# Optimization experiments

Hardware: AMD Instinct MI355X
Metric: run time of the kernel (lower is better)

The kernel has to match this reference:

```python
import jax, jax.numpy as jnp
import numpy as np

B, T, K = 128, 1024, 24
START_TAG, END_TAG = 22, 23


def setup_inputs() -> dict:
    key = jax.random.key(0)
    k1, k2, k3 = jax.random.split(key, 3)
    scores = jax.random.normal(k1, (B, T, K, K), dtype=jnp.float32)
    targets = jax.random.randint(k2, (B, T), 0, K * K)
    # lengths must be sorted descending (pack_padded_sequence convention), >= 1
    lengths = jnp.sort(jax.random.randint(k3, (B,), 1, T + 1))[::-1]
    return {"scores": scores, "targets": targets, "lengths": lengths}


def reference(scores, targets, lengths):
    b, t_len, k, _ = scores.shape
    # gold path score: gather targets from flattened [B,T,K*K] view, mask by length
    flat = scores.reshape(b, t_len, k * k)
    scores_at_targets = jnp.take_along_axis(flat, targets[:, :, None], axis=2)[..., 0]  # [B,T]
    time_mask = jnp.arange(t_len)[None, :] < lengths[:, None]  # [B,T]
    gold_score = jnp.sum(jnp.where(time_mask, scores_at_targets, 0.0))

    # CRF forward recursion (log-sum-exp over previous tag), sequential over time.
    # t == 0: initialize with row of the <start> tag (all lengths >= 1).
    prev = scores[:, 0, START_TAG, :]  # [B,K]

    def step(prev, inp):
        s_t, m_t = inp  # s_t: [B,K,K], m_t: [B] bool (t < length)
        new = jax.scipy.special.logsumexp(s_t + prev[:, :, None], axis=1)  # [B,K]
        prev = jnp.where(m_t[:, None], new, prev)
        return prev, None

    s_rest = jnp.moveaxis(scores[:, 1:], 0, 1)  # time-major [T-1,B,K,K]
    m_rest = jnp.arange(1, t_len)[:, None] < lengths[None, :]  # [T-1,B]
    prev, _ = jax.lax.scan(step, prev, (s_rest, m_rest))

    all_paths_scores = prev[:, END_TAG].sum()
    return (all_paths_scores - gold_score) / b
```

## Files before the change

kernel.cpp:

```cpp
#include <hip/hip_runtime.h>

static constexpr int T_LEN = 1024;
static constexpr int KTAG = 24;
static constexpr int MAT = 576;
static constexpr int START_TAG = 22;
static constexpr int END_TAG = 23;
static constexpr int BATCH = 128;
static constexpr int CHUNK = 32;
static constexpr int NCHUNK = 32;

static constexpr float LOG2E = 1.4426950408889634f;
static constexpr float LN2   = 0.6931471805599453f;

typedef short  bf16x8 __attribute__((ext_vector_type(8)));
typedef float  f32x16 __attribute__((ext_vector_type(16)));

__device__ __forceinline__ float fexp2(float x) { return __builtin_amdgcn_exp2f(x); }
__device__ __forceinline__ float flog2(float x) { return __builtin_amdgcn_logf(x); }

__device__ __forceinline__ unsigned int f2bf(float x) {
  unsigned int u = __float_as_uint(x);
  u += 0x7FFFu + ((u >> 16) & 1u);
  return u >> 16;
}

__global__ __launch_bounds__(256) void chunkprod_kernel(
    const float* __restrict__ scores, const int* __restrict__ targets,
    const int* __restrict__ lengths,
    float* __restrict__ wsP, int* __restrict__ wsE, float* __restrict__ wsG)
{
  const int widx = threadIdx.x >> 6;
  const int lane = threadIdx.x & 63;
  const int i = blockIdx.x * 4 + widx;
  const int pr = i >> 1;
  const int anti = i & 1;
  const int b0 = pr >> 4;
  const int c0 = pr & 15;
  const int b = anti ? (127 - b0) : b0;
  const int c = anti ? (31 - c0) : c0;
  const int len = lengths[b];
  const int t0 = 1 + c * CHUNK;
  if (t0 >= len) return;
  const int n = min(CHUNK, len - t0);
  const int hd = lane >> 5;
  const int m = lane & 31;
  const int mc = m < KTAG ? m : KTAG - 1;
  const float* sb = scores + (size_t)b * T_LEN * MAT;

  {
    float gs = 0.f;
    if (lane < n) {
      int t = t0 + lane;
      gs = sb[(size_t)t * MAT + targets[b * T_LEN + t]];
    }
    #pragma unroll
    for (int off = 1; off < 64; off <<= 1) gs += __shfl_xor(gs, off, 64);
    if (lane == 0) wsG[b * NCHUNK + c] = gs;
  }

  int off1[8], off2[4];
  #pragma unroll
  for (int e = 0; e < 8; ++e) {
    int k = (e & 3) + 8 * (e >> 2) + 4 * hd;
    off1[e] = k * KTAG + mc;
  }
  #pragma unroll
  for (int e = 0; e < 4; ++e) {
    int k = 16 + e + 4 * hd;
    off2[e] = k * KTAG + mc;
  }

  float b0r[12], b1r[12], b2r[12], b3r[12];
  auto LOADA = [&](float (&buf)[12], int step) {
    const float* pb = sb + (size_t)(t0 + step) * MAT;
    #pragma unroll
    for (int e = 0; e < 8; ++e) buf[e] = pb[off1[e]];
    #pragma unroll
    for (int e = 0; e < 4; ++e) buf[8 + e] = pb[off2[e]];
  };

  unsigned int p[8];
  #pragma unroll
  for (int r = 0; r < 8; ++r) {
    int rlo = ((2 * r) & 3) + 8 * ((2 * r) >> 2) + 4 * hd;
    unsigned int v = 0;
    if (m == rlo)     v |= 0x3F80u;
    if (m == rlo + 1) v |= (0x3F80u << 16);
    p[r] = v;
  }

  int E = 0;

  auto STEPM = [&](const float (&buf)[12]) -> f32x16 {
    float av[12];
    #pragma unroll
    for (int i2 = 0; i2 < 12; ++i2) av[i2] = fexp2(buf[i2] * LOG2E);
    bf16x8 a1, a2;
    #pragma unroll
    for (int e = 0; e < 8; ++e) a1[e] = (short)f2bf(av[e]);
    #pragma unroll
    for (int e = 0; e < 4; ++e) a2[e] = (short)f2bf(av[8 + e]);
    #pragma unroll
    for (int e = 4; e < 8; ++e) a2[e] = 0;
    union { unsigned int u[4]; bf16x8 v; } B1, B2;
    B1.u[0] = p[0]; B1.u[1] = p[1]; B1.u[2] = p[2]; B1.u[3] = p[3];
    B2.u[0] = p[4]; B2.u[1] = p[5]; B2.u[2] = p[6]; B2.u[3] = p[7];
    f32x16 d = {};
    d = __builtin_amdgcn_mfma_f32_32x32x16_bf16(a1, B1.v, d, 0, 0, 0);
    d = __builtin_amdgcn_mfma_f32_32x32x16_bf16(a2, B2.v, d, 0, 0, 0);
    return d;
  };

  auto CONV = [&](const f32x16& d) {
    int rb = __builtin_amdgcn_readfirstlane(__float_as_int(d[0]));
    int dd = ((rb >> 23) & 255) - 127;
    E += dd;
    float sc = __int_as_float((127 - dd) << 23);
    #pragma unroll
    for (int r = 0; r < 8; ++r)
      p[r] = (f2bf(d[2 * r + 1] * sc) << 16) | f2bf(d[2 * r] * sc);
  };

  LOADA(b0r, 0);
  LOADA(b1r, n > 1 ? 1 : 0);
  LOADA(b2r, n > 2 ? 2 : 0);
  LOADA(b3r, n > 3 ? 3 : 0);
  f32x16 z;
  int s = 0;
  for (;;) {
    z = STEPM(b0r);
    if (s + 1 >= n) break;
    CONV(z); { int t = s + 4; LOADA(b0r, t < n ? t : n - 1); }
    z = STEPM(b1r);
    if (s + 2 >= n) break;
    CONV(z); { int t = s + 5; LOADA(b1r, t < n ? t : n - 1); }
    z = STEPM(b2r);
    if (s + 3 >= n) break;
    CONV(z); { int t = s + 6; LOADA(b2r, t < n ? t : n - 1); }
    z = STEPM(b3r);
    if (s + 4 >= n) break;
    CONV(z); { int t = s + 7; LOADA(b3r, t < n ? t : n - 1); }
    s += 4;
  }

  if (m < KTAG) {
    float* dst = wsP + (size_t)(b * NCHUNK + c) * MAT + m * KTAG;
    float4 v0 = make_float4(z[0], z[1], z[2],  z[3]);
    float4 v1 = make_float4(z[4], z[5], z[6],  z[7]);
    float4 v2 = make_float4(z[8], z[9], z[10], z[11]);
    *(float4*)(dst + 4 * hd)      = v0;
    *(float4*)(dst + 8 + 4 * hd)  = v1;
    *(float4*)(dst + 16 + 4 * hd) = v2;
  }
  if (lane == 0) wsE[b * NCHUNK + c] = E;
}

__global__ __launch_bounds__(64) void chainmat_kernel(
    const float* __restrict__ scores, const int* __restrict__ targets,
    const float* __restrict__ wsP, const int* __restrict__ wsE,
    const float* __restrict__ wsG, const int* __restrict__ lengths,
    float* __restrict__ wsR)
{
  const int b = blockIdx.x;
  const int lane = threadIdx.x;
  const int hd = lane >> 5;
  const int m = lane & 31;
  const int mc = m < KTAG ? m : KTAG - 1;
  const int len = lengths[b];
  const int nc = (len + 30) >> 5;
  const float* sb = scores + (size_t)b * T_LEN * MAT;

  float gv = 0.f;
  if (lane < nc) gv = wsG[b * NCHUNK + lane];
  #pragma unroll
  for (int off = 1; off < 64; off <<= 1) gv += __shfl_xor(gv, off, 64);
  const float g0 = sb[targets[b * T_LEN]];

  if (nc == 0) {
    if (lane == 0) wsR[b] = sb[START_TAG * KTAG + END_TAG] - g0;
    return;
  }

  int ev = 0;
  if (lane < nc) ev = wsE[b * NCHUNK + lane];
  #pragma unroll
  for (int off = 1; off < 64; off <<= 1) ev += __shfl_xor(ev, off, 64);
  int E = ev;

  int off1[8], off2[4];
  #pragma unroll
  for (int e = 0; e < 8; ++e) {
    int k = (e & 3) + 8 * (e >> 2) + 4 * hd;
    off1[e] = k * KTAG + mc;
  }
  #pragma unroll
  for (int e = 0; e < 4; ++e) {
    int k = 16 + e + 4 * hd;
    off2[e] = k * KTAG + mc;
  }
  const float* pbase = wsP + (size_t)b * NCHUNK * MAT;

  float b0[12], b1[12];
  auto LOADP = [&](float (&buf)[12], int c) {
    const float* pb = pbase + (size_t)c * MAT;
    #pragma unroll
    for (int e = 0; e < 8; ++e) buf[e] = pb[off1[e]];
    #pragma unroll
    for (int e = 0; e < 4; ++e) buf[8 + e] = pb[off2[e]];
  };

  unsigned int p[8];
  #pragma unroll
  for (int r = 0; r < 8; ++r) {
    int rlo = ((2 * r) & 3) + 8 * ((2 * r) >> 2) + 4 * hd;
    unsigned int v = 0;
    if (m == rlo)     v |= 0x3F80u;
    if (m == rlo + 1) v |= (0x3F80u << 16);
    p[r] = v;
  }

  auto STEPP = [&](const float (&buf)[12]) -> f32x16 {
    bf16x8 a1, a2;
    #pragma unroll
    for (int e = 0; e < 8; ++e) a1[e] = (short)f2bf(buf[e]);
    #pragma unroll
    for (int e = 0; e < 4; ++e) a2[e] = (short)f2bf(buf[8 + e]);
    #pragma unroll
    for (int e = 4; e < 8; ++e) a2[e] = 0;
    union { unsigned int u[4]; bf16x8 v; } B1, B2;
    B1.u[0] = p[0]; B1.u[1] = p[1]; B1.u[2] = p[2]; B1.u[3] = p[3];
    B2.u[0] = p[4]; B2.u[1] = p[5]; B2.u[2] = p[6]; B2.u[3] = p[7];
    f32x16 d = {};
    d = __builtin_amdgcn_mfma_f32_32x32x16_bf16(a1, B1.v, d, 0, 0, 0);
    d = __builtin_amdgcn_mfma_f32_32x32x16_bf16(a2, B2.v, d, 0, 0, 0);
    return d;
  };
  auto CONVP = [&](const f32x16& d) {
    int rb = __builtin_amdgcn_readfirstlane(__float_as_int(d[0]));
    int dd = ((rb >> 23) & 255) - 127;
    E += dd;
    float sc = __int_as_float((127 - dd) << 23);
    #pragma unroll
    for (int r = 0; r < 8; ++r)
      p[r] = (f2bf(d[2 * r + 1] * sc) << 16) | f2bf(d[2 * r] * sc);
  };

  LOADP(b0, 0);
  LOADP(b1, nc > 1 ? 1 : 0);
  f32x16 z;
  int c = 0;
  for (;;) {
    z = STEPP(b0);
    if (c + 1 >= nc) break;
    CONVP(z); { int t = c + 2; LOADP(b0, t < nc ? t : nc - 1); }
    z = STEPP(b1);
    if (c + 2 >= nc) break;
    CONVP(z); { int t = c + 3; LOADP(b1, t < nc ? t : nc - 1); }
    c += 2;
  }

  float tau0 = fexp2(sb[START_TAG * KTAG + mc] * LOG2E);
  float v = (hd == 1 && m < KTAG) ? z[11] * tau0 : 0.f;
  #pragma unroll
  for (int off = 1; off < 64; off <<= 1) v += __shfl_xor(v, off, 64);
  if (lane == 0) {
    float logZ = ((float)E + flog2(v)) * LN2;
    wsR[b] = logZ - gv - g0;
  }
}

__global__ __launch_bounds__(64) void sum_kernel(
    const float* __restrict__ wsR, float* __restrict__ out)
{
  const int lane = threadIdx.x;
  float v = wsR[lane] + wsR[lane + 64];
  #pragma unroll
  for (int off = 1; off < 64; off <<= 1) v += __shfl_xor(v, off, 64);
  if (lane == 0) out[0] = v * (1.0f / (float)BATCH);
}

template<int DIR>
__device__ __forceinline__ int run_chain(const float* __restrict__ base, int len, int n,
                                         volatile float* __restrict__ tau,
                                         int lane, int h, int jj)
{
  int E = 0;
  float ref = 1.0f;
  float A[12], B[12], Cb[12];
  auto LOAD = [&](float (&buf)[12], int i) {
    if (DIR == 0) {
      const float* p = base + (size_t)(1 + i) * MAT + h * 12 * KTAG + jj;
      #pragma unroll
      for (int k = 0; k < 12; ++k) buf[k] = p[k * KTAG];
    } else {
      const float4* p = (const float4*)(base + (size_t)(len - 1 - i) * MAT + jj * KTAG + h * 12);
      float4 x = p[0], y = p[1], z = p[2];
      buf[0]=x.x; buf[1]=x.y; buf[2]=x.z; buf[3]=x.w;
      buf[4]=y.x; buf[5]=y.y; buf[6]=y.z; buf[7]=y.w;
      buf[8]=z.x; buf[9]=z.y; buf[10]=z.z; buf[11]=z.w;
    }
  };
  auto STEP = [&](const float (&buf)[12]) {
    int rb = __builtin_amdgcn_readfirstlane(__float_as_int(ref));
    int d = ((rb >> 23) & 255) - 127;
    float sc = __int_as_float((127 - d) << 23);
    E += d;
    float w[12];
    #pragma unroll
    for (int k = 0; k < 12; ++k) w[k] = fexp2(buf[k] * LOG2E);
    const float4* tp = (const float4*)((const float*)&tau[h * 12]);
    float4 t0 = tp[0], t1 = tp[1], t2 = tp[2];
    float a0 = t0.x*w[0], a1 = t0.y*w[1], a2 = t0.z*w[2], a3 = t0.w*w[3];
    a0 = fmaf(t1.x, w[4],  a0); a1 = fmaf(t1.y, w[5],  a1);
    a2 = fmaf(t1.z, w[6],  a2); a3 = fmaf(t1.w, w[7],  a3);
    a0 = fmaf(t2.x, w[8],  a0); a1 = fmaf(t2.y, w[9],  a1);
    a2 = fmaf(t2.z, w[10], a2); a3 = fmaf(t2.w, w[11], a3);
    float part = (a0 + a1) + (a2 + a3);
    float tot = part + __shfl_xor(part, 32, 64);
    float tn = tot * sc;
    if (lane < KTAG) tau[lane] = tn;
    ref = tn;
  };
  if (n > 0) {
    LOAD(A, 0); LOAD(B, n > 1 ? 1 : 0); LOAD(Cb, n > 2 ? 2 : 0);
    int i = 0;
    while (i + 3 <= n) {
      STEP(A);  { int ii = i + 3; LOAD(A,  ii < n ? ii : n - 1); }
      STEP(B);  { int ii = i + 4; LOAD(B,  ii < n ? ii : n - 1); }
      STEP(Cb); { int ii = i + 5; LOAD(Cb, ii < n ? ii : n - 1); }
      i += 3;
    }
    if (i < n)     STEP(A);
    if (i + 1 < n) STEP(B);
  }
  return E;
}

__global__ __launch_bounds__(128) void crf_fb_kernel(
    const float* __restrict__ scores, const int* __restrict__ lengths,
    float* __restrict__ acc)
{
  __shared__ float sm[2][32];
  __shared__ int smE[2];
  const int b = blockIdx.x;
  const int tid = threadIdx.x;
  const int wid = tid >> 6;
  const int lane = tid & 63;
  const int h = lane >> 5;
  const int j = lane & 31;
  const int jj = j < KTAG ? j : KTAG - 1;
  const int len = lengths[b];
  const float* base = scores + (size_t)b * T_LEN * MAT;
  const int m = len >> 1;
  volatile float* tau = sm[wid];
  int E;
  if (wid == 0) {
    if (lane < KTAG) tau[lane] = fexp2(base[START_TAG * KTAG + lane] * LOG2E);
    E = run_chain<0>(base, len, m, tau, lane, h, jj);
  } else {
    if (lane < KTAG) tau[lane] = (lane == END_TAG) ? 1.0f : 0.0f;
    E = run_chain<1>(base, len, len - 1 - m, tau, lane, h, jj);
  }
  if (lane == 0) smE[wid] = E;
  __syncthreads();
  if (wid == 0) {
    float v = (lane < KTAG) ? sm[0][lane] * sm[1][lane] : 0.0f;
    #pragma unroll
    for (int off = 1; off < 32; off <<= 1) v += __shfl_xor(v, off, 64);
    if (lane == 0) {
      float res = ((float)(smE[0] + smE[1]) + flog2(v)) * LN2;
      atomicAdd(acc, res);
    }
  }
}

__global__ __launch_bounds__(256) void gold_kernel(
    const float* __restrict__ scores, const int* __restrict__ targets,
    const int* __restrict__ lengths, float* __restrict__ acc)
{
  const int idx = blockIdx.x * blockDim.x + threadIdx.x;
  const int b = idx >> 10;
  const int t = idx & (T_LEN - 1);
  float v = 0.f;
  if (t < lengths[b]) v = scores[(size_t)idx * MAT + targets[idx]];
  #pragma unroll
  for (int off = 1; off < 64; off <<= 1) v += __shfl_xor(v, off, 64);
  if ((threadIdx.x & 63) == 0) atomicAdd(acc, -v);
}

__global__ void finalize_kernel(const float* __restrict__ acc, float* __restrict__ out) {
  out[0] = acc[0] * (1.0f / (float)BATCH);
}

extern "C" void kernel_launch(void* const* d_in, const int* in_sizes, int n_in,
                              void* d_out, int out_size, void* d_ws, size_t ws_size,
                              hipStream_t stream) {
  const float* scores = (const float*)d_in[0];
  const int* targets  = (const int*)d_in[1];
  const int* lengths  = (const int*)d_in[2];
  float* out = (float*)d_out;

  const size_t pbytes = (size_t)BATCH * NCHUNK * MAT * sizeof(float);
  const size_t ebytes = (size_t)BATCH * NCHUNK * sizeof(int);
  const size_t gbytes = (size_t)BATCH * NCHUNK * sizeof(float);
  const size_t need = pbytes + ebytes + gbytes + BATCH * sizeof(float);

  if (ws_size >= need) {
    float* wsP = (float*)d_ws;
    int*   wsE = (int*)((char*)d_ws + pbytes);
    float* wsG = (float*)((char*)d_ws + pbytes + ebytes);
    float* wsR = (float*)((char*)d_ws + pbytes + ebytes + gbytes);
    chunkprod_kernel<<<BATCH * NCHUNK / 4, 256, 0, stream>>>(scores, targets, lengths,
                                                             wsP, wsE, wsG);
    chainmat_kernel<<<BATCH, 64, 0, stream>>>(scores, targets, wsP, wsE, wsG,
                                              lengths, wsR);
    sum_kernel<<<1, 64, 0, stream>>>(wsR, out);
  } else {
    float* acc = (float*)d_ws;
    hipMemsetAsync(acc, 0, sizeof(float), stream);
    gold_kernel<<<BATCH * T_LEN / 256, 256, 0, stream>>>(scores, targets, lengths, acc);
    crf_fb_kernel<<<BATCH, 128, 0, stream>>>(scores, lengths, acc);
    finalize_kernel<<<1, 1, 0, stream>>>(acc, out);
  }
}
```

Before: 55.14 us.

## Fuse chunk products, chain, and sum into one kernel via atomic last-block counters

Result: slower. 144.3 us (+161.7%).

```diff
diff --git a/kernel.cpp b/kernel.cpp
--- a/kernel.cpp
+++ b/kernel.cpp
@@ -24,39 +24,32 @@
   return u >> 16;
 }
 
-__global__ __launch_bounds__(256) void chunkprod_kernel(
+__global__ __launch_bounds__(256) void fused_kernel(
     const float* __restrict__ scores, const int* __restrict__ targets,
     const int* __restrict__ lengths,
-    float* __restrict__ wsP, int* __restrict__ wsE, float* __restrict__ wsG)
+    float* __restrict__ wsP, int* __restrict__ wsE, float* __restrict__ wsG,
+    float* __restrict__ wsR, int* __restrict__ cntA, int* __restrict__ cntB,
+    float* __restrict__ out)
 {
   const int widx = threadIdx.x >> 6;
   const int lane = threadIdx.x & 63;
   const int i = blockIdx.x * 4 + widx;
   const int pr = i >> 1;
   const int anti = i & 1;
-  const int b0 = pr >> 4;
-  const int c0 = pr & 15;
-  const int b = anti ? (127 - b0) : b0;
-  const int c = anti ? (31 - c0) : c0;
+  const int b0i = pr >> 4;
+  const int c0i = pr & 15;
+  const int b = anti ? (127 - b0i) : b0i;
+  const int c = anti ? (31 - c0i) : c0i;
   const int len = lengths[b];
   const int t0 = 1 + c * CHUNK;
-  if (t0 >= len) return;
-  const int n = min(CHUNK, len - t0);
+  const bool live = t0 < len;
+  if (!live && c != 0) return;
+  const int nc = (len + 30) >> 5;
+  const int T = nc > 0 ? nc : 1;
   const int hd = lane >> 5;
   const int m = lane & 31;
   const int mc = m < KTAG ? m : KTAG - 1;
   const float* sb = scores + (size_t)b * T_LEN * MAT;
-
-  {
-    float gs = 0.f;
-    if (lane < n) {
-      int t = t0 + lane;
-      gs = sb[(size_t)t * MAT + targets[b * T_LEN + t]];
-    }
-    #pragma unroll
-    for (int off = 1; off < 64; off <<= 1) gs += __shfl_xor(gs, off, 64);
-    if (lane == 0) wsG[b * NCHUNK + c] = gs;
-  }
 
   int off1[8], off2[4];
   #pragma unroll
@@ -70,209 +63,198 @@
     off2[e] = k * KTAG + mc;
   }
 
-  float b0r[12], b1r[12], b2r[12], b3r[12];
-  auto LOADA = [&](float (&buf)[12], int step) {
-    const float* pb = sb + (size_t)(t0 + step) * MAT;
-    #pragma unroll
-    for (int e = 0; e < 8; ++e) buf[e] = pb[off1[e]];
-    #pragma unroll
-    for (int e = 0; e < 4; ++e) buf[8 + e] = pb[off2[e]];
-  };
-
-  unsigned int p[8];
-  #pragma unroll
-  for (int r = 0; r < 8; ++r) {
-    int rlo = ((2 * r) & 3) + 8 * ((2 * r) >> 2) + 4 * hd;
-    unsigned int v = 0;
-    if (m == rlo)     v |= 0x3F80u;
-    if (m == rlo + 1) v |= (0x3F80u << 16);
-    p[r] = v;
-  }
-
-  int E = 0;
-
-  auto STEPM = [&](const float (&buf)[12]) -> f32x16 {
-    float av[12];
-    #pragma unroll
-    for (int i2 = 0; i2 < 12; ++i2) av[i2] = fexp2(buf[i2] * LOG2E);
-    bf16x8 a1, a2;
-    #pragma unroll
-    for (int e = 0; e < 8; ++e) a1[e] = (short)f2bf(av[e]);
-    #pragma unroll
-    for (int e = 0; e < 4; ++e) a2[e] = (short)f2bf(av[8 + e]);
-    #pragma unroll
-    for (int e = 4; e < 8; ++e) a2[e] = 0;
-    union { unsigned int u[4]; bf16x8 v; } B1, B2;
-    B1.u[0] = p[0]; B1.u[1] = p[1]; B1.u[2] = p[2]; B1.u[3] = p[3];
-    B2.u[0] = p[4]; B2.u[1] = p[5]; B2.u[2] = p[6]; B2.u[3] = p[7];
-    f32x16 d = {};
-    d = __builtin_amdgcn_mfma_f32_32x32x16_bf16(a1, B1.v, d, 0, 0, 0);
-    d = __builtin_amdgcn_mfma_f32_32x32x16_bf16(a2, B2.v, d, 0, 0, 0);
-    return d;
-  };
-
-  auto CONV = [&](const f32x16& d) {
-    int rb = __builtin_amdgcn_readfirstlane(__float_as_int(d[0]));
-    int dd = ((rb >> 23) & 255) - 127;
-    E += dd;
-    float sc = __int_as_float((127 - dd) << 23);
-    #pragma unroll
-    for (int r = 0; r < 8; ++r)
-      p[r] = (f2bf(d[2 * r + 1] * sc) << 16) | f2bf(d[2 * r] * sc);
-  };
-
-  LOADA(b0r, 0);
-  LOADA(b1r, n > 1 ? 1 : 0);
-  LOADA(b2r, n > 2 ? 2 : 0);
-  LOADA(b3r, n > 3 ? 3 : 0);
-  f32x16 z;
-  int s = 0;
-  for (;;) {
-    z = STEPM(b0r);
-    if (s + 1 >= n) break;
-    CONV(z); { int t = s + 4; LOADA(b0r, t < n ? t : n - 1); }
-    z = STEPM(b1r);
-    if (s + 2 >= n) break;
-    CONV(z); { int t = s + 5; LOADA(b1r, t < n ? t : n - 1); }
-    z = STEPM(b2r);
-    if (s + 3 >= n) break;
-    CONV(z); { int t = s + 6; LOADA(b2r, t < n ? t : n - 1); }
-    z = STEPM(b3r);
-    if (s + 4 >= n) break;
-    CONV(z); { int t = s + 7; LOADA(b3r, t < n ? t : n - 1); }
-    s += 4;
-  }
-
-  if (m < KTAG) {
-    float* dst = wsP + (size_t)(b * NCHUNK + c) * MAT + m * KTAG;
-    float4 v0 = make_float4(z[0], z[1], z[2],  z[3]);
-    float4 v1 = make_float4(z[4], z[5], z[6],  z[7]);
-    float4 v2 = make_float4(z[8], z[9], z[10], z[11]);
-    *(float4*)(dst + 4 * hd)      = v0;
-    *(float4*)(dst + 8 + 4 * hd)  = v1;
-    *(float4*)(dst + 16 + 4 * hd) = v2;
-  }
-  if (lane == 0) wsE[b * NCHUNK + c] = E;
-}
-
-__global__ __launch_bounds__(64) void chainmat_kernel(
-    const float* __restrict__ scores, const int* __restrict__ targets,
-    const float* __restrict__ wsP, const int* __restrict__ wsE,
-    const float* __restrict__ wsG, const int* __restrict__ lengths,
-    float* __restrict__ wsR)
-{
-  const int b = blockIdx.x;
-  const int lane = threadIdx.x;
-  const int hd = lane >> 5;
-  const int m = lane & 31;
-  const int mc = m < KTAG ? m : KTAG - 1;
-  const int len = lengths[b];
-  const int nc = (len + 30) >> 5;
-  const float* sb = scores + (size_t)b * T_LEN * MAT;
-
-  float gv = 0.f;
-  if (lane < nc) gv = wsG[b * NCHUNK + lane];
-  #pragma unroll
-  for (int off = 1; off < 64; off <<= 1) gv += __shfl_xor(gv, off, 64);
+  if (live) {
+    const int n = min(CHUNK, len - t0);
+
+    {
+      float gs = 0.f;
+      if (lane < n) {
+        int t = t0 + lane;
+        gs = sb[(size_t)t * MAT + targets[b * T_LEN + t]];
+      }
+      #pragma unroll
+      for (int off = 1; off < 64; off <<= 1) gs += __shfl_xor(gs, off, 64);
+      if (lane == 0) wsG[b * NCHUNK + c] = gs;
+    }
+
+    float b0r[12], b1r[12], b2r[12], b3r[12];
+    auto LOADA = [&](float (&buf)[12], int step) {
+      const float* pb = sb + (size_t)(t0 + step) * MAT;
+      #pragma unroll
+      for (int e = 0; e < 8; ++e) buf[e] = pb[off1[e]];
+      #pragma unroll
+      for (int e = 0; e < 4; ++e) buf[8 + e] = pb[off2[e]];
+    };
+
+    unsigned int p[8];
+    #pragma unroll
+    for (int r = 0; r < 8; ++r) {
+      int rlo = ((2 * r) & 3) + 8 * ((2 * r) >> 2) + 4 * hd;
+      unsigned int v = 0;
+      if (m == rlo)     v |= 0x3F80u;
+      if (m == rlo + 1) v |= (0x3F80u << 16);
+      p[r] = v;
+    }
+
+    int E = 0;
+    auto STEPM = [&](const float (&buf)[12]) -> f32x16 {
+      float av[12];
+      #pragma unroll
+      for (int q = 0; q < 12; ++q) av[q] = fexp2(buf[q] * LOG2E);
+      bf16x8 a1, a2;
+      #pragma unroll
+      for (int e = 0; e < 8; ++e) a1[e] = (short)f2bf(av[e]);
+      #pragma unroll
+      for (int e = 0; e < 4; ++e) a2[e] = (short)f2bf(av[8 + e]);
+      #pragma unroll
+      for (int e = 4; e < 8; ++e) a2[e] = 0;
+      union { unsigned int u[4]; bf16x8 v; } B1, B2;
+      B1.u[0] = p[0]; B1.u[1] = p[1]; B1.u[2] = p[2]; B1.u[3] = p[3];
+      B2.u[0] = p[4]; B2.u[1] = p[5]; B2.u[2] = p[6]; B2.u[3] = p[7];
+      f32x16 d = {};
+      d = __builtin_amdgcn_mfma_f32_32x32x16_bf16(a1, B1.v, d, 0, 0, 0);
+      d = __builtin_amdgcn_mfma_f32_32x32x16_bf16(a2, B2.v, d, 0, 0, 0);
+      return d;
+    };
+    auto CONV = [&](const f32x16& d) {
+      int rb = __builtin_amdgcn_readfirstlane(__float_as_int(d[0]));
+      int dd = ((rb >> 23) & 255) - 127;
+      E += dd;
+      float sc = __int_as_float((127 - dd) << 23);
+      #pragma unroll
+      for (int r = 0; r < 8; ++r)
+        p[r] = (f2bf(d[2 * r + 1] * sc) << 16) | f2bf(d[2 * r] * sc);
+    };
+
+    LOADA(b0r, 0);
+    LOADA(b1r, n > 1 ? 1 : 0);
+    LOADA(b2r, n > 2 ? 2 : 0);
+    LOADA(b3r, n > 3 ? 3 : 0);
+    f32x16 z;
+    int s = 0;
+    for (;;) {
+      z = STEPM(b0r);
+      if (s + 1 >= n) break;
+      CONV(z); { int t = s + 4; LOADA(b0r, t < n ? t : n - 1); }
+      z = STEPM(b1r);
+      if (s + 2 >= n) break;
+      CONV(z); { int t = s + 5; LOADA(b1r, t < n ? t : n - 1); }
+      z = STEPM(b2r);
+      if (s + 3 >= n) break;
+      CONV(z); { int t = s + 6; LOADA(b2r, t < n ? t : n - 1); }
+      z = STEPM(b3r);
+      if (s + 4 >= n) break;
+      CONV(z); { int t = s + 7; LOADA(b3r, t < n ? t : n - 1); }
+      s += 4;
+    }
+
+    if (m < KTAG) {
+      float* dst = wsP + (size_t)(b * NCHUNK + c) * MAT + m * KTAG;
+      *(float4*)(dst + 4 * hd)      = make_float4(z[0], z[1], z[2],  z[3]);
+      *(float4*)(dst + 8 + 4 * hd)  = make_float4(z[4], z[5], z[6],  z[7]);
+      *(float4*)(dst + 16 + 4 * hd) = make_float4(z[8], z[9], z[10], z[11]);
+    }
+    if (lane == 0) wsE[b * NCHUNK + c] = E;
+  }
+
+  __threadfence();
+  int old = 0;
+  if (lane == 0) old = atomicAdd(&cntA[b], 1);
+  old = __shfl(old, 0, 64);
+  if (old != T - 1) return;
+  __threadfence();
+
   const float g0 = sb[targets[b * T_LEN]];
-
   if (nc == 0) {
     if (lane == 0) wsR[b] = sb[START_TAG * KTAG + END_TAG] - g0;
-    return;
-  }
-
-  int ev = 0;
-  if (lane < nc) ev = wsE[b * NCHUNK + lane];
-  #pragma unroll
-  for (int off = 1; off < 64; off <<= 1) ev += __shfl_xor(ev, off, 64);
-  int E = ev;
-
-  int off1[8], off2[4];
-  #pragma unroll
-  for (int e = 0; e < 8; ++e) {
-    int k = (e & 3) + 8 * (e >> 2) + 4 * hd;
-    off1[e] = k * KTAG + mc;
-  }
-  #pragma unroll
-  for (int e = 0; e < 4; ++e) {
-    int k = 16 + e + 4 * hd;
-    off2[e] = k * KTAG + mc;
-  }
-  const float* pbase = wsP + (size_t)b * NCHUNK * MAT;
-
-  float b0[12], b1[12];
-  auto LOADP = [&](float (&buf)[12], int c) {
-    const float* pb = pbase + (size_t)c * MAT;
-    #pragma unroll
-    for (int e = 0; e < 8; ++e) buf[e] = pb[off1[e]];
-    #pragma unroll
-    for (int e = 0; e < 4; ++e) buf[8 + e] = pb[off2[e]];
-  };
-
-  unsigned int p[8];
-  #pragma unroll
-  for (int r = 0; r < 8; ++r) {
-    int rlo = ((2 * r) & 3) + 8 * ((2 * r) >> 2) + 4 * hd;
-    unsigned int v = 0;
-    if (m == rlo)     v |= 0x3F80u;
-    if (m == rlo + 1) v |= (0x3F80u << 16);
-    p[r] = v;
-  }
-
-  auto STEPP = [&](const float (&buf)[12]) -> f32x16 {
-    bf16x8 a1, a2;
-    #pragma unroll
-    for (int e = 0; e < 8; ++e) a1[e] = (short)f2bf(buf[e]);
-    #pragma unroll
-    for (int e = 0; e < 4; ++e) a2[e] = (short)f2bf(buf[8 + e]);
-    #pragma unroll
-    for (int e = 4; e < 8; ++e) a2[e] = 0;
-    union { unsigned int u[4]; bf16x8 v; } B1, B2;
-    B1.u[0] = p[0]; B1.u[1] = p[1]; B1.u[2] = p[2]; B1.u[3] = p[3];
-    B2.u[0] = p[4]; B2.u[1] = p[5]; B2.u[2] = p[6]; B2.u[3] = p[7];
-    f32x16 d = {};
-    d = __builtin_amdgcn_mfma_f32_32x32x16_bf16(a1, B1.v, d, 0, 0, 0);
-    d = __builtin_amdgcn_mfma_f32_32x32x16_bf16(a2, B2.v, d, 0, 0, 0);
-    return d;
-  };
-  auto CONVP = [&](const f32x16& d) {
-    int rb = __builtin_amdgcn_readfirstlane(__float_as_int(d[0]));
-    int dd = ((rb >> 23) & 255) - 127;
-    E += dd;
-    float sc = __int_as_float((127 - dd) << 23);
-    #pragma unroll
-    for (int r = 0; r < 8; ++r)
-      p[r] = (f2bf(d[2 * r + 1] * sc) << 16) | f2bf(d[2 * r] * sc);
-  };
-
-  LOADP(b0, 0);
-  LOADP(b1, nc > 1 ? 1 : 0);
-  f32x16 z;
-  int c = 0;
-  for (;;) {
-    z = STEPP(b0);
-    if (c + 1 >= nc) break;
-    CONVP(z); { int t = c + 2; LOADP(b0, t < nc ? t : nc - 1); }
-    z = STEPP(b1);
-    if (c + 2 >= nc) break;
-    CONVP(z); { int t = c + 3; LOADP(b1, t < nc ? t : nc - 1); }
-    c += 2;
-  }
-
-  float tau0 = fexp2(sb[START_TAG * KTAG + mc] * LOG2E);
-  float v = (hd == 1 && m < KTAG) ? z[11] * tau0 : 0.f;
-  #pragma unroll
-  for (int off = 1; off < 64; off <<= 1) v += __shfl_xor(v, off, 64);
-  if (lane == 0) {
-    float logZ = ((float)E + flog2(v)) * LN2;
-    wsR[b] = logZ - gv - g0;
-  }
-}
-
-__global__ __launch_bounds__(64) void sum_kernel(
-    const float* __restrict__ wsR, float* __restrict__ out)
-{
-  const int lane = threadIdx.x;
+  } else {
+    float gv = 0.f;
+    if (lane < nc) gv = wsG[b * NCHUNK + lane];
+    #pragma unroll
+    for (int off = 1; off < 64; off <<= 1) gv += __shfl_xor(gv, off, 64);
+
+    int ev = 0;
+    if (lane < nc) ev = wsE[b * NCHUNK + lane];
+    #pragma unroll
+    for (int off = 1; off < 64; off <<= 1) ev += __shfl_xor(ev, off, 64);
+    int E = ev;
+
+    const float* pbase = wsP + (size_t)b * NCHUNK * MAT;
+    float f0[12], f1[12];
+    auto LOADP = [&](float (&buf)[12], int cc) {
+      const float* pb = pbase + (size_t)cc * MAT;
+      #pragma unroll
+      for (int e = 0; e < 8; ++e) buf[e] = pb[off1[e]];
+      #pragma unroll
+      for (int e = 0; e < 4; ++e) buf[8 + e] = pb[off2[e]];
+    };
+
+    unsigned int p[8];
+    #pragma unroll
+    for (int r = 0; r < 8; ++r) {
+      int rlo = ((2 * r) & 3) + 8 * ((2 * r) >> 2) + 4 * hd;
+      unsigned int v = 0;
+      if (m == rlo)     v |= 0x3F80u;
+      if (m == rlo + 1) v |= (0x3F80u << 16);
+      p[r] = v;
+    }
+
+    auto STEPP = [&](const float (&buf)[12]) -> f32x16 {
+      bf16x8 a1, a2;
+      #pragma unroll
+      for (int e = 0; e < 8; ++e) a1[e] = (short)f2bf(buf[e]);
+      #pragma unroll
+      for (int e = 0; e < 4; ++e) a2[e] = (short)f2bf(buf[8 + e]);
+      #pragma unroll
+      for (int e = 4; e < 8; ++e) a2[e] = 0;
+      union { unsigned int u[4]; bf16x8 v; } B1, B2;
+      B1.u[0] = p[0]; B1.u[1] = p[1]; B1.u[2] = p[2]; B1.u[3] = p[3];
+      B2.u[0] = p[4]; B2.u[1] = p[5]; B2.u[2] = p[6]; B2.u[3] = p[7];
+      f32x16 d = {};
+      d = __builtin_amdgcn_mfma_f32_32x32x16_bf16(a1, B1.v, d, 0, 0, 0);
+      d = __builtin_amdgcn_mfma_f32_32x32x16_bf16(a2, B2.v, d, 0, 0, 0);
+      return d;
+    };
+    auto CONVP = [&](const f32x16& d) {
+      int rb = __builtin_amdgcn_readfirstlane(__float_as_int(d[0]));
+      int dd = ((rb >> 23) & 255) - 127;
+      E += dd;
+      float sc = __int_as_float((127 - dd) << 23);
+      #pragma unroll
+      for (int r = 0; r < 8; ++r)
+        p[r] = (f2bf(d[2 * r + 1] * sc) << 16) | f2bf(d[2 * r] * sc);
+    };
+
+    LOADP(f0, 0);
+    LOADP(f1, nc > 1 ? 1 : 0);
+    f32x16 z;
+    int cc = 0;
+    for (;;) {
+      z = STEPP(f0);
+      if (cc + 1 >= nc) break;
+      CONVP(z); { int t = cc + 2; LOADP(f0, t < nc ? t : nc - 1); }
+      z = STEPP(f1);
+      if (cc + 2 >= nc) break;
+      CONVP(z); { int t = cc + 3; LOADP(f1, t < nc ? t : nc - 1); }
+      cc += 2;
+    }
+
+    float tau0 = fexp2(sb[START_TAG * KTAG + mc] * LOG2E);
+    float v = (hd == 1 && m < KTAG) ? z[11] * tau0 : 0.f;
+    #pragma unroll
+    for (int off = 1; off < 64; off <<= 1) v += __shfl_xor(v, off, 64);
+    if (lane == 0) {
+      float logZ = ((float)E + flog2(v)) * LN2;
+      wsR[b] = logZ - gv - g0;
+    }
+  }
+
+  __threadfence();
+  int old2 = 0;
+  if (lane == 0) old2 = atomicAdd(cntB, 1);
+  old2 = __shfl(old2, 0, 64);
+  if (old2 != BATCH - 1) return;
+  __threadfence();
   float v = wsR[lane] + wsR[lane + 64];
   #pragma unroll
   for (int off = 1; off < 64; off <<= 1) v += __shfl_xor(v, off, 64);
@@ -403,18 +385,21 @@
   const size_t pbytes = (size_t)BATCH * NCHUNK * MAT * sizeof(float);
   const size_t ebytes = (size_t)BATCH * NCHUNK * sizeof(int);
   const size_t gbytes = (size_t)BATCH * NCHUNK * sizeof(float);
-  const size_t need = pbytes + ebytes + gbytes + BATCH * sizeof(float);
+  const size_t rbytes = (size_t)BATCH * sizeof(float);
+  const size_t cbytes = (size_t)BATCH * sizeof(int) + 64;
+  const size_t need = pbytes + ebytes + gbytes + rbytes + cbytes;
 
   if (ws_size >= need) {
-    float* wsP = (float*)d_ws;
-    int*   wsE = (int*)((char*)d_ws + pbytes);
-    float* wsG = (float*)((char*)d_ws + pbytes + ebytes);
-    float* wsR = (float*)((char*)d_ws + pbytes + ebytes + gbytes);
-    chunkprod_kernel<<<BATCH * NCHUNK / 4, 256, 0, stream>>>(scores, targets, lengths,
-                                                             wsP, wsE, wsG);
-    chainmat_kernel<<<BATCH, 64, 0, stream>>>(scores, targets, wsP, wsE, wsG,
-                                              lengths, wsR);
-    sum_kernel<<<1, 64, 0, stream>>>(wsR, out);
+    char* base = (char*)d_ws;
+    float* wsP = (float*)base;
+    int*   wsE = (int*)(base + pbytes);
+    float* wsG = (float*)(base + pbytes + ebytes);
+    float* wsR = (float*)(base + pbytes + ebytes + gbytes);
+    int*   cntA = (int*)(base + pbytes + ebytes + gbytes + rbytes);
+    int*   cntB = cntA + BATCH;
+    hipMemsetAsync(cntA, 0, cbytes, stream);
+    fused_kernel<<<BATCH * NCHUNK / 4, 256, 0, stream>>>(
+        scores, targets, lengths, wsP, wsE, wsG, wsR, cntA, cntB, out);
   } else {
     float* acc = (float*)d_ws;
     hipMemsetAsync(acc, 0, sizeof(float), stream);
```
